# Performance work log

Measured on AMD Instinct MI355X. Metric: run time of the kernel, lower is better.

## Reference

```python
import jax, jax.numpy as jnp
import numpy as np

D, T, B, DEPTH, WIN, H = 1024, 2048, 4, 2, 128, 4
HD = D // H


def setup_inputs() -> dict:
    key = jax.random.key(0)
    ks = iter(jax.random.split(key, 32))
    s = D ** -0.5
    inp = {
        'x': jax.random.normal(next(ks), (B, T, D), jnp.float32),
        'ln1_s': jnp.ones((DEPTH, D)), 'ln1_b': jnp.zeros((DEPTH, D)),
        'ln2_s': jnp.ones((DEPTH, D)), 'ln2_b': jnp.zeros((DEPTH, D)),
        'ln3_s': jnp.ones((DEPTH, D)), 'ln3_b': jnp.zeros((DEPTH, D)),
        'rg_in_w': jax.random.normal(next(ks), (DEPTH, D, D)) * s,
        'rg_in_b': jnp.zeros((DEPTH, D)),
        'rg_gate_w': jax.random.normal(next(ks), (DEPTH, D, D)) * s,
        'rg_gate_b': jnp.zeros((DEPTH, D)),
        'rg_out_w': jax.random.normal(next(ks), (DEPTH, D, D)) * s,
        'rg_out_b': jnp.zeros((DEPTH, D)),
        'qkv_w': jax.random.normal(next(ks), (DEPTH, D, 3 * D)) * s,
        'qkv_b': jnp.zeros((DEPTH, 3 * D)),
        'attn_out_w': jax.random.normal(next(ks), (DEPTH, D, D)) * s,
        'attn_out_b': jnp.zeros((DEPTH, D)),
        'mlp_w1': jax.random.normal(next(ks), (DEPTH, D, 4 * D)) * s,
        'mlp_b1': jnp.zeros((DEPTH, 4 * D)),
        'mlp_w2': jax.random.normal(next(ks), (DEPTH, 4 * D, D)) * (4 * D) ** -0.5,
        'mlp_b2': jnp.zeros((DEPTH, D)),
    }
    return inp


def _ln(x, s, b):
    m = x.mean(-1, keepdims=True)
    v = ((x - m) ** 2).mean(-1, keepdims=True)
    return (x - m) / jnp.sqrt(v + 1e-5) * s + b


def _rg_lru(x, wi, bi, wg, bg, wo, bo):
    u = x @ wi + bi                      # [B,T,D]
    g = jax.nn.sigmoid(x @ wg + bg)      # [B,T,D]
    # h_t = g_t * h_{t-1} + (1-g_t) * u_t, h_{-1}=0 -> log-depth associative scan
    def comb(l, r):
        return (l[0] * r[0], r[0] * l[1] + r[1])
    _, h = jax.lax.associative_scan(comb, (g, (1.0 - g) * u), axis=1)
    return h @ wo + bo


def _local_attn(x, wqkv, bqkv, wo, bo):
    b, t, d = x.shape
    qkv = (x @ wqkv + bqkv).reshape(b, t, 3, H, HD)
    qkv = jnp.transpose(qkv, (2, 0, 3, 1, 4))  # [3,B,H,T,hd]
    q, k, v = qkv[0], qkv[1], qkv[2]
    scores = jnp.einsum('bhid,bhjd->bhij', q, k) / (HD ** 0.5)
    i = jnp.arange(t)[:, None]
    j = jnp.arange(t)[None, :]
    mask = (j <= i) & (j >= i - (WIN - 1))
    scores = jnp.where(mask, scores, -jnp.inf)
    p = jax.nn.softmax(scores, axis=-1)
    y = jnp.einsum('bhij,bhjd->bhid', p, v)
    y = jnp.transpose(y, (0, 2, 1, 3)).reshape(b, t, d)
    return y @ wo + bo


def reference(x, ln1_s, ln1_b, ln2_s, ln2_b, ln3_s, ln3_b,
              rg_in_w, rg_in_b, rg_gate_w, rg_gate_b, rg_out_w, rg_out_b,
              qkv_w, qkv_b, attn_out_w, attn_out_b,
              mlp_w1, mlp_b1, mlp_w2, mlp_b2):
    for l in range(DEPTH):
        x = x + _rg_lru(_ln(x, ln1_s[l], ln1_b[l]),
                        rg_in_w[l], rg_in_b[l], rg_gate_w[l], rg_gate_b[l],
                        rg_out_w[l], rg_out_b[l])
        x = x + _local_attn(_ln(x, ln2_s[l], ln2_b[l]),
                            qkv_w[l], qkv_b[l], attn_out_w[l], attn_out_b[l])
        h = _ln(x, ln3_s[l], ln3_b[l])
        h = jax.nn.gelu(h @ mlp_w1[l] + mlp_b1[l], approximate=False) @ mlp_w2[l] + mlp_b2[l]
        x = x + h
    return x
```

## Files before the change

### kernel.cpp

```cpp
#include <hip/hip_runtime.h>
#include <math.h>

#define DD 1024
#define TT 2048
#define BB 4
#define HH 4
#define HDIM 256
#define NLAYER 2
#define MM (BB*TT)
#define NCHUNK 32
#define CHUNK (TT/NCHUNK)

typedef unsigned short u16;
typedef __bf16 bf16x8 __attribute__((ext_vector_type(8)));
typedef float f32x4 __attribute__((ext_vector_type(4)));

__device__ __forceinline__ float b2f(u16 h) {
  unsigned u = ((unsigned)h) << 16;
  return __builtin_bit_cast(float, u);
}
__device__ __forceinline__ u16 f2b(float f) {
  unsigned u = __builtin_bit_cast(unsigned, f);
  u += 0x7fffu + ((u >> 16) & 1u);
  return (u16)(u >> 16);
}

#define GLD16(g, l) __builtin_amdgcn_global_load_lds( \
    (__attribute__((address_space(1))) void*)(void*)(g), \
    (__attribute__((address_space(3))) void*)(l), 16, 0, 0)

__device__ __forceinline__ void wg_barrier() {
  asm volatile("" ::: "memory");
  __builtin_amdgcn_s_barrier();
  asm volatile("" ::: "memory");
}
template<int N> __device__ __forceinline__ void wait_vmcnt() {
  asm volatile("s_waitcnt vmcnt(%0)" :: "i"(N) : "memory");
}

__global__ __launch_bounds__(256)
void transpose_cvt(const float* __restrict__ W, u16* __restrict__ Wt, int K, int N) {
  __shared__ float tile[32][33];
  const int n0 = blockIdx.x << 5, k0 = blockIdx.y << 5;
  const int tx = threadIdx.x, ty = threadIdx.y;
#pragma unroll
  for (int i = 0; i < 4; ++i)
    tile[ty + i*8][tx] = W[(size_t)(k0 + ty + i*8) * N + n0 + tx];
  __syncthreads();
#pragma unroll
  for (int i = 0; i < 4; ++i)
    Wt[(size_t)(n0 + ty + i*8) * K + k0 + tx] = f2b(tile[tx][ty + i*8]);
}

__global__ __launch_bounds__(256)
void ln_k(const float* __restrict__ x, const float* __restrict__ sc,
          const float* __restrict__ bi, u16* __restrict__ xn) {
  const int row = blockIdx.x;
  const int tid = threadIdx.x;
  const float4 xv = ((const float4*)(x + (size_t)row * DD))[tid];
  float s = xv.x + xv.y + xv.z + xv.w;
  float q = xv.x*xv.x + xv.y*xv.y + xv.z*xv.z + xv.w*xv.w;
#pragma unroll
  for (int o = 1; o < 64; o <<= 1) { s += __shfl_xor(s, o); q += __shfl_xor(q, o); }
  __shared__ float rs[4], rq[4];
  if ((tid & 63) == 0) { rs[tid >> 6] = s; rq[tid >> 6] = q; }
  __syncthreads();
  s = rs[0] + rs[1] + rs[2] + rs[3];
  q = rq[0] + rq[1] + rq[2] + rq[3];
  const float mean = s * (1.f / DD);
  const float var = q * (1.f / DD) - mean * mean;
  const float rstd = rsqrtf(var + 1e-5f);
  const float4 sv = ((const float4*)sc)[tid];
  const float4 bv = ((const float4*)bi)[tid];
  const u16 o0 = f2b((xv.x - mean) * rstd * sv.x + bv.x);
  const u16 o1 = f2b((xv.y - mean) * rstd * sv.y + bv.y);
  const u16 o2 = f2b((xv.z - mean) * rstd * sv.z + bv.z);
  const u16 o3 = f2b((xv.w - mean) * rstd * sv.w + bv.w);
  uint2 pk;
  pk.x = (unsigned)o0 | ((unsigned)o1 << 16);
  pk.y = (unsigned)o2 | ((unsigned)o3 << 16);
  *(uint2*)(xn + (size_t)row * DD + (tid << 2)) = pk;
}

template<int EPI, int BN>
__global__ __launch_bounds__(512)
void gemm256t(const u16* __restrict__ A, const u16* __restrict__ Wt,
              const float* __restrict__ bias, const float* __restrict__ bias2,
              float* __restrict__ outf, u16* __restrict__ outb, int K, int N) {
  constexpr int NI = BN / 64;
  constexpr int PAIR = 2 + BN / 128;
  extern __shared__ u16 lds[];
  u16* Al = lds;
  u16* Bl = lds + 32768;
  const int tid = threadIdx.x;
  const int gx = gridDim.x;
  const int nwg = gx * (int)gridDim.y;
  int lid = (int)blockIdx.y * gx + (int)blockIdx.x;
  lid = (lid & 7) * (nwg >> 3) + (lid >> 3);
  const int m0 = (lid / gx) << 8;
  const int n0 = (lid % gx) * BN;
  const int lane = tid & 63;
  const int wid = tid >> 6;
  const int wm = wid >> 2;
  const int wn = wid & 3;
  const int g = lane >> 4;
  const int lc = lane & 15;
  const int rkey = (lc >> 1) & 3;
  const int q = tid >> 2;
  const int sslot = tid & 3;
  const int skey = (q >> 1) & 3;
  const int scs = (sslot ^ skey) << 3;

  auto stage_pair = [&](int kt, int buf, int ch) {
    const int kbase = (kt << 6) + (ch << 5);
#pragma unroll
    for (int i = 0; i < 2; ++i) {
      const int row = i*128 + q;
      GLD16(A + (size_t)(m0 + row) * K + kbase + scs,
            Al + buf*16384 + ch*8192 + i*4096 + tid*8);
    }
#pragma unroll
    for (int i = 0; i < BN/128; ++i) {
      const int row = i*128 + q;
      GLD16(Wt + (size_t)(n0 + row) * K + kbase + scs,
            Bl + buf*(BN*64) + ch*(BN*32) + i*4096 + tid*8);
    }
  };

  f32x4 acc[8][NI];
#pragma unroll
  for (int i = 0; i < 8; ++i)
#pragma unroll
    for (int j = 0; j < NI; ++j)
#pragma unroll
      for (int e = 0; e < 4; ++e) acc[i][j][e] = 0.f;

  const int KT = K >> 6;
  stage_pair(0, 0, 0);
  stage_pair(0, 0, 1);

  for (int kt = 0; kt < KT; ++kt) {
    const int cur = kt & 1;
    const bool more = (kt + 1 < KT);
#pragma unroll
    for (int kk = 0; kk < 2; ++kk) {
      if (kk == 0) wait_vmcnt<PAIR>();
      else if (more) wait_vmcnt<PAIR>();
      else wait_vmcnt<0>();
      wg_barrier();
      const int so = (g ^ rkey) << 3;
      const u16* Ab = Al + cur*16384 + kk*8192;
      const u16* Bb = Bl + cur*(BN*64) + kk*(BN*32);
      bf16x8 bfr[NI];
#pragma unroll
      for (int ni = 0; ni < NI; ++ni)
        bfr[ni] = *(const bf16x8*)(Bb + (wn*(NI*16) + ni*16 + lc)*32 + so);
      bf16x8 af0[4];
#pragma unroll
      for (int i = 0; i < 4; ++i)
        af0[i] = *(const bf16x8*)(Ab + (wm*128 + i*16 + lc)*32 + so);
      if (more) stage_pair(kt + 1, cur ^ 1, kk);
      __builtin_amdgcn_s_setprio(1);
#pragma unroll
      for (int i = 0; i < 4; ++i)
#pragma unroll
        for (int ni = 0; ni < NI; ++ni)
          acc[i][ni] = __builtin_amdgcn_mfma_f32_16x16x32_bf16(af0[i], bfr[ni], acc[i][ni], 0, 0, 0);
      __builtin_amdgcn_s_setprio(0);
      bf16x8 af1[4];
#pragma unroll
      for (int i = 0; i < 4; ++i)
        af1[i] = *(const bf16x8*)(Ab + (wm*128 + 64 + i*16 + lc)*32 + so);
      __builtin_amdgcn_s_setprio(1);
#pragma unroll
      for (int i = 0; i < 4; ++i)
#pragma unroll
        for (int ni = 0; ni < NI; ++ni)
          acc[4 + i][ni] = __builtin_amdgcn_mfma_f32_16x16x32_bf16(af1[i], bfr[ni], acc[4 + i][ni], 0, 0, 0);
      __builtin_amdgcn_s_setprio(0);
    }
    wg_barrier();
  }

#pragma unroll
  for (int mi = 0; mi < 8; ++mi) {
#pragma unroll
    for (int ni = 0; ni < NI; ++ni) {
      const int n = n0 + wn*(NI*16) + ni*16 + lc;
      const int mbase = m0 + wm*128 + (mi & 3)*16 + (mi >> 2)*64 + (g << 2);
      if (EPI == 4) {
        const float bia = bias[n];
        if (n < 2048) {
#pragma unroll
          for (int e = 0; e < 4; ++e)
            outb[(size_t)(mbase + e) * 2048 + n] = f2b(acc[mi][ni][e] + bia);
        } else {
          const int hh = (n - 2048) >> 8, dim = (n - 2048) & 255;
          const int bidx = mbase >> 11, t = mbase & 2047;
          const u16 a0 = f2b(acc[mi][ni][0] + bia);
          const u16 a1 = f2b(acc[mi][ni][1] + bia);
          const u16 a2 = f2b(acc[mi][ni][2] + bia);
          const u16 a3 = f2b(acc[mi][ni][3] + bia);
          uint2 pk;
          pk.x = (unsigned)a0 | ((unsigned)a1 << 16);
          pk.y = (unsigned)a2 | ((unsigned)a3 << 16);
          u16* vtp = (u16*)outf;
          *(uint2*)(vtp + ((size_t)((bidx*4 + hh)*256 + dim)) * 2048 + t) = pk;
        }
      } else if (EPI == 5) {
        const float bia = (n < 1024) ? bias[n] : bias2[n - 1024];
        u16* dst = (n < 1024) ? outb : (u16*)outf;
        const int nn = n & 1023;
#pragma unroll
        for (int e = 0; e < 4; ++e)
          dst[(size_t)(mbase + e) * 1024 + nn] = f2b(acc[mi][ni][e] + bia);
      } else if (EPI == 2) {
        const float bia = bias[n];
#pragma unroll
        for (int e = 0; e < 4; ++e) {
          const float v = acc[mi][ni][e] + bia;
          const float zc = fminf(fmaxf(1.5957691216f * (v + 0.044715f*v*v*v), -30.f), 30.f);
          outb[(size_t)(mbase + e) * N + n] = f2b(v / (1.f + __expf(-zc)));
        }
      } else {
        const float bia = bias[n];
#pragma unroll
        for (int e = 0; e < 4; ++e)
          outf[(size_t)(mbase + e) * N + n] += acc[mi][ni][e] + bia;
      }
    }
  }
}

__global__ __launch_bounds__(256)
void scan1_k(const u16* __restrict__ zpre, const u16* __restrict__ u,
             float* __restrict__ aggA, float* __restrict__ aggB) {
  const int d = blockIdx.x * 256 + threadIdx.x;
  const int c = blockIdx.y, b = blockIdx.z;
  const size_t base = ((size_t)b * TT + (size_t)c * CHUNK) * DD + d;
  float a = 1.f, acc = 0.f;
  for (int t = 0; t < CHUNK; ++t) {
    const float gl = 1.f / (1.f + __expf(-b2f(zpre[base + (size_t)t * DD])));
    const float ul = b2f(u[base + (size_t)t * DD]);
    acc = gl * acc + (1.f - gl) * ul;
    a *= gl;
  }
  const size_t o = ((size_t)b * NCHUNK + c) * DD + d;
  aggA[o] = a; aggB[o] = acc;
}

__global__ __launch_bounds__(256)
void scan2_k(const float* __restrict__ aggA, const float* __restrict__ aggB,
             float* __restrict__ carry) {
  const int idx = blockIdx.x * 256 + threadIdx.x;
  const int b = idx >> 10, d = idx & 1023;
  float h = 0.f;
  for (int c = 0; c < NCHUNK; ++c) {
    const size_t o = ((size_t)b * NCHUNK + c) * DD + d;
    carry[o] = h;
    h = aggA[o] * h + aggB[o];
  }
}

__global__ __launch_bounds__(256)
void scan3_k(const u16* __restrict__ zpre, const u16* __restrict__ u,
             const float* __restrict__ carry, u16* __restrict__ hout) {
  const int d = blockIdx.x * 256 + threadIdx.x;
  const int c = blockIdx.y, b = blockIdx.z;
  const size_t base = ((size_t)b * TT + (size_t)c * CHUNK) * DD + d;
  float h = carry[((size_t)b * NCHUNK + c) * DD + d];
  for (int t = 0; t < CHUNK; ++t) {
    const float gl = 1.f / (1.f + __expf(-b2f(zpre[base + (size_t)t * DD])));
    const float ul = b2f(u[base + (size_t)t * DD]);
    h = gl * h + (1.f - gl) * ul;
    hout[base + (size_t)t * DD] = f2b(h);
  }
}

__global__ __launch_bounds__(256)
void attn_mfma(const u16* __restrict__ qkb, const u16* __restrict__ vt,
               u16* __restrict__ y) {
  __shared__ u16 kv[16384];
  __shared__ u16 pb[4][16][200];
  const int tid = threadIdx.x;
  const int lane = tid & 63;
  const int wid = tid >> 6;
  const int g = lane >> 4;
  const int lc = lane & 15;
  const int t0 = blockIdx.x << 6;
  const int bh = blockIdx.y;
  const int bT = (bh >> 2) * TT;
  const int h = bh & 3;

  bf16x8 afq[8];
  {
    const u16* qg = qkb + (size_t)(bT + t0 + wid*16 + lc) * 2048 + h*256 + g*8;
#pragma unroll
    for (int ks = 0; ks < 8; ++ks)
      afq[ks] = __builtin_bit_cast(bf16x8, *(const uint4*)(qg + ks*32));
  }

  f32x4 sc[12];
#pragma unroll
  for (int f = 0; f < 12; ++f)
#pragma unroll
    for (int e = 0; e < 4; ++e) sc[f][e] = 0.f;

  const int koff = 1024 + h*256;
#pragma unroll
  for (int c = 0; c < 3; ++c) {
    const int j0 = t0 + (c - 2) * 64;
    if (j0 < 0) {
#pragma unroll
      for (int nt = 0; nt < 4; ++nt)
#pragma unroll
        for (int e = 0; e < 4; ++e) sc[c*4+nt][e] = -1e30f;
      continue;
    }
    __syncthreads();
    {
      const u16* kg = qkb + (size_t)(bT + j0) * 2048 + koff;
#pragma unroll
      for (int i = 0; i < 8; ++i) {
        const int o16 = i*256 + tid;
        const int slab = o16 >> 8, key = (o16 >> 2) & 63, ds = o16 & 3;
        GLD16(kg + (size_t)key*2048 + slab*32 + ds*8, kv + o16*8);
      }
    }
    __syncthreads();
#pragma unroll
    for (int nt = 0; nt < 4; ++nt) {
      f32x4 s = sc[c*4+nt];
#pragma unroll
      for (int ks = 0; ks < 8; ++ks) {
        const bf16x8 kb = *(const bf16x8*)(kv + ks*2048 + (nt*16 + lc)*32 + g*8);
        s = __builtin_amdgcn_mfma_f32_16x16x32_bf16(afq[ks], kb, s, 0, 0, 0);
      }
      sc[c*4+nt] = s;
    }
#pragma unroll
    for (int nt = 0; nt < 4; ++nt)
#pragma unroll
      for (int e = 0; e < 4; ++e) {
        const int tl = wid*16 + g*4 + e;
        const int jl = nt*16 + lc;
        const bool ok = (c == 1) || (c == 2 ? (jl <= tl) : (jl >= tl + 1));
        sc[c*4+nt][e] = ok ? sc[c*4+nt][e] * 0.0625f : -1e30f;
      }
  }

#pragma unroll
  for (int e = 0; e < 4; ++e) {
    float m = -1e30f;
#pragma unroll
    for (int f = 0; f < 12; ++f) m = fmaxf(m, sc[f][e]);
    m = fmaxf(m, __shfl_xor(m, 1)); m = fmaxf(m, __shfl_xor(m, 2));
    m = fmaxf(m, __shfl_xor(m, 4)); m = fmaxf(m, __shfl_xor(m, 8));
    float s = 0.f;
#pragma unroll
    for (int f = 0; f < 12; ++f) { const float p = __expf(sc[f][e] - m); sc[f][e] = p; s += p; }
    s += __shfl_xor(s, 1); s += __shfl_xor(s, 2);
    s += __shfl_xor(s, 4); s += __shfl_xor(s, 8);
    const float is = 1.f / s;
#pragma unroll
    for (int f = 0; f < 12; ++f) sc[f][e] *= is;
  }
#pragma unroll
  for (int c = 0; c < 3; ++c)
#pragma unroll
    for (int nt = 0; nt < 4; ++nt)
#pragma unroll
      for (int e = 0; e < 4; ++e)
        pb[wid][g*4 + e][c*64 + nt*16 + lc] = f2b(sc[c*4+nt][e]);

  f32x4 acc[16];
#pragma unroll
  for (int nt = 0; nt < 16; ++nt)
#pragma unroll
    for (int e = 0; e < 4; ++e) acc[nt][e] = 0.f;

  const u16* vg = vt + (size_t)bh * 256 * 2048;
#pragma unroll
  for (int c = 0; c < 3; ++c) {
    const int j0 = t0 + (c - 2) * 64;
    if (j0 < 0) continue;
    __syncthreads();
#pragma unroll
    for (int i = 0; i < 8; ++i) {
      const int o16 = i*256 + tid;
      const int dim = o16 >> 3, slot = o16 & 7;
      const int ss = slot ^ (dim & 7);
      GLD16(vg + (size_t)dim*2048 + j0 + ss*8, kv + o16*8);
    }
    __syncthreads();
#pragma unroll
    for (int ks = 0; ks < 2; ++ks) {
      const bf16x8 pa = *(const bf16x8*)&pb[wid][lc][(c*2 + ks)*32 + g*8];
#pragma unroll
      for (int nt = 0; nt < 16; ++nt) {
        const int dim = nt*16 + lc;
        int boff = dim*128 + ks*64 + g*16;
        boff ^= (dim & 7) << 4;
        const bf16x8 vb = *(const bf16x8*)((const char*)kv + boff);
        acc[nt] = __builtin_amdgcn_mfma_f32_16x16x32_bf16(pa, vb, acc[nt], 0, 0, 0);
      }
    }
  }

#pragma unroll
  for (int nt = 0; nt < 16; ++nt)
#pragma unroll
    for (int e = 0; e < 4; ++e) {
      const int tok = bT + t0 + wid*16 + g*4 + e;
      y[(size_t)tok * 1024 + h*256 + nt*16 + lc] = f2b(acc[nt][e]);
    }
}

extern "C" void kernel_launch(void* const* d_in, const int* in_sizes, int n_in,
                              void* d_out, int out_size, void* d_ws, size_t ws_size,
                              hipStream_t stream) {
  const float* x_in      = (const float*)d_in[0];
  const float* ln1_s     = (const float*)d_in[1];
  const float* ln1_b     = (const float*)d_in[2];
  const float* ln2_s     = (const float*)d_in[3];
  const float* ln2_b     = (const float*)d_in[4];
  const float* ln3_s     = (const float*)d_in[5];
  const float* ln3_b     = (const float*)d_in[6];
  const float* rg_in_w   = (const float*)d_in[7];
  const float* rg_in_b   = (const float*)d_in[8];
  const float* rg_gate_w = (const float*)d_in[9];
  const float* rg_gate_b = (const float*)d_in[10];
  const float* rg_out_w  = (const float*)d_in[11];
  const float* rg_out_b  = (const float*)d_in[12];
  const float* qkv_w     = (const float*)d_in[13];
  const float* qkv_b     = (const float*)d_in[14];
  const float* attn_out_w= (const float*)d_in[15];
  const float* attn_out_b= (const float*)d_in[16];
  const float* mlp_w1    = (const float*)d_in[17];
  const float* mlp_b1    = (const float*)d_in[18];
  const float* mlp_w2    = (const float*)d_in[19];
  const float* mlp_b2    = (const float*)d_in[20];

  hipFuncSetAttribute((const void*)&gemm256t<5,256>, hipFuncAttributeMaxDynamicSharedMemorySize, 131072);
  hipFuncSetAttribute((const void*)&gemm256t<4,256>, hipFuncAttributeMaxDynamicSharedMemorySize, 131072);
  hipFuncSetAttribute((const void*)&gemm256t<2,256>, hipFuncAttributeMaxDynamicSharedMemorySize, 131072);
  hipFuncSetAttribute((const void*)&gemm256t<3,128>, hipFuncAttributeMaxDynamicSharedMemorySize, 98304);

  float* x = (float*)d_out;
  char* ws = (char*)d_ws;
  u16*  wt     = (u16*)ws;
  u16*  xn     = (u16*)(ws + 62914560);
  char* bigS   = ws + 62914560 + 16777216;
  char* smallS = bigS + 67108864;
  float* aggA  = (float*)(smallS + 16777216);
  float* aggB  = aggA + (size_t)BB * NCHUNK * DD;
  float* carry = aggB + (size_t)BB * NCHUNK * DD;

  u16* ubuf = (u16*)bigS;
  u16* zbuf = (u16*)(bigS + 33554432);
  u16* qkb  = (u16*)bigS;
  u16* vtb  = (u16*)(bigS + 33554432);
  u16* hid  = (u16*)bigS;
  u16* hbuf = (u16*)smallS;
  u16* ybuf = (u16*)smallS;

  hipMemcpyAsync(x, x_in, (size_t)MM * DD * sizeof(float), hipMemcpyDeviceToDevice, stream);

  const size_t LW = 15728640;
  const dim3 tb(32, 8);
  for (int l = 0; l < NLAYER; ++l) {
    u16* base = wt + (size_t)l * LW;
    transpose_cvt<<<dim3(32, 32),  tb, 0, stream>>>(rg_in_w   + (size_t)l*DD*DD,   base + 0,        DD, DD);
    transpose_cvt<<<dim3(32, 32),  tb, 0, stream>>>(rg_gate_w + (size_t)l*DD*DD,   base + 1048576,  DD, DD);
    transpose_cvt<<<dim3(32, 32),  tb, 0, stream>>>(rg_out_w  + (size_t)l*DD*DD,   base + 2097152,  DD, DD);
    transpose_cvt<<<dim3(96, 32),  tb, 0, stream>>>(qkv_w     + (size_t)l*DD*3072, base + 3145728,  DD, 3072);
    transpose_cvt<<<dim3(32, 32),  tb, 0, stream>>>(attn_out_w+ (size_t)l*DD*DD,   base + 6291456,  DD, DD);
    transpose_cvt<<<dim3(128, 32), tb, 0, stream>>>(mlp_w1    + (size_t)l*DD*4096, base + 7340032,  DD, 4096);
    transpose_cvt<<<dim3(32, 128), tb, 0, stream>>>(mlp_w2    + (size_t)l*4096*DD, base + 11534336, 4096, DD);
  }

  for (int l = 0; l < NLAYER; ++l) {
    u16* base = wt + (size_t)l * LW;
    ln_k<<<MM, 256, 0, stream>>>(x, ln1_s + l*DD, ln1_b + l*DD, xn);
    gemm256t<5,256><<<dim3(8, 32), 512, 131072, stream>>>(xn, base + 0, rg_in_b + l*DD, rg_gate_b + l*DD,
                                                          (float*)zbuf, ubuf, DD, 2048);
    scan1_k<<<dim3(4, NCHUNK, BB), 256, 0, stream>>>(zbuf, ubuf, aggA, aggB);
    scan2_k<<<16, 256, 0, stream>>>(aggA, aggB, carry);
    scan3_k<<<dim3(4, NCHUNK, BB), 256, 0, stream>>>(zbuf, ubuf, carry, hbuf);
    gemm256t<3,128><<<dim3(8, 32), 512, 98304, stream>>>(hbuf, base + 2097152, rg_out_b + l*DD, nullptr,
                                                         x, nullptr, DD, 1024);
    ln_k<<<MM, 256, 0, stream>>>(x, ln2_s + l*DD, ln2_b + l*DD, xn);
    gemm256t<4,256><<<dim3(12, 32), 512, 131072, stream>>>(xn, base + 3145728, qkv_b + l*3072, nullptr,
                                                           (float*)vtb, qkb, DD, 3072);
    attn_mfma<<<dim3(TT/64, BB*HH), 256, 0, stream>>>(qkb, vtb, ybuf);
    gemm256t<3,128><<<dim3(8, 32), 512, 98304, stream>>>(ybuf, base + 6291456, attn_out_b + l*DD, nullptr,
                                                         x, nullptr, DD, 1024);
    ln_k<<<MM, 256, 0, stream>>>(x, ln3_s + l*DD, ln3_b + l*DD, xn);
    gemm256t<2,256><<<dim3(16, 32), 512, 131072, stream>>>(xn, base + 7340032, mlp_b1 + l*4096, nullptr,
                                                           nullptr, hid, DD, 4096);
    gemm256t<3,128><<<dim3(8, 32), 512, 98304, stream>>>(hid, base + 11534336, mlp_b2 + l*DD, nullptr,
                                                         x, nullptr, 4096, 1024);
  }
}
```

Measured before the change: 910.5 us.

## Software-pipeline GEMM LDS fragment reads one K-half ahead with deeper prefetch

Restructures the GEMM main loop around K half-chunks. It prefetches three global stages up front and loads the A0/B register fragments for the next half-chunk before running the MFMAs of the current one, using double-buffered register sets. It also drops the trailing per-iteration barrier. The aim is to hide LDS read latency and global load waits behind MFMA work, at the cost of more VGPRs and a more delicate buffer-reuse and barrier ordering.

```diff
diff --git a/kernel.cpp b/kernel.cpp
--- a/kernel.cpp
+++ b/kernel.cpp
@@ -110,8 +110,10 @@
   const int sslot = tid & 3;
   const int skey = (q >> 1) & 3;
   const int scs = (sslot ^ skey) << 3;
-
-  auto stage_pair = [&](int kt, int buf, int ch) {
+  const int so = (g ^ rkey) << 3;
+
+  auto stage_pairP = [&](int p) {
+    const int kt = p >> 1, buf = kt & 1, ch = p & 1;
     const int kbase = (kt << 6) + (ch << 5);
 #pragma unroll
     for (int i = 0; i < 2; ++i) {
@@ -126,6 +128,24 @@
             Bl + buf*(BN*64) + ch*(BN*32) + i*4096 + tid*8);
     }
   };
+  auto read_b = [&](int p, bf16x8* bf) {
+    const u16* Bb = Bl + ((p >> 1) & 1)*(BN*64) + (p & 1)*(BN*32);
+#pragma unroll
+    for (int ni = 0; ni < NI; ++ni)
+      bf[ni] = *(const bf16x8*)(Bb + (wn*(NI*16) + ni*16 + lc)*32 + so);
+  };
+  auto read_a0 = [&](int p, bf16x8* af) {
+    const u16* Ab = Al + ((p >> 1) & 1)*16384 + (p & 1)*8192;
+#pragma unroll
+    for (int i = 0; i < 4; ++i)
+      af[i] = *(const bf16x8*)(Ab + (wm*128 + i*16 + lc)*32 + so);
+  };
+  auto read_a1 = [&](int p, bf16x8* af) {
+    const u16* Ab = Al + ((p >> 1) & 1)*16384 + (p & 1)*8192;
+#pragma unroll
+    for (int i = 0; i < 4; ++i)
+      af[i] = *(const bf16x8*)(Ab + (wm*128 + 64 + i*16 + lc)*32 + so);
+  };
 
   f32x4 acc[8][NI];
 #pragma unroll
@@ -136,50 +156,58 @@
       for (int e = 0; e < 4; ++e) acc[i][j][e] = 0.f;
 
   const int KT = K >> 6;
-  stage_pair(0, 0, 0);
-  stage_pair(0, 0, 1);
-
-  for (int kt = 0; kt < KT; ++kt) {
-    const int cur = kt & 1;
-    const bool more = (kt + 1 < KT);
-#pragma unroll
-    for (int kk = 0; kk < 2; ++kk) {
-      if (kk == 0) wait_vmcnt<PAIR>();
-      else if (more) wait_vmcnt<PAIR>();
-      else wait_vmcnt<0>();
+  const int NP = KT << 1;
+  stage_pairP(0); stage_pairP(1); stage_pairP(2);
+  wait_vmcnt<2*PAIR>();
+  wg_barrier();
+  bf16x8 afX[4], bfX[NI], afY[4], bfY[NI], af1[4];
+  read_a0(0, afX); read_b(0, bfX);
+
+  for (int P = 0; P < NP; P += 2) {
+    {
+      if (P + 2 < NP) wait_vmcnt<PAIR>(); else wait_vmcnt<0>();
       wg_barrier();
-      const int so = (g ^ rkey) << 3;
-      const u16* Ab = Al + cur*16384 + kk*8192;
-      const u16* Bb = Bl + cur*(BN*64) + kk*(BN*32);
-      bf16x8 bfr[NI];
-#pragma unroll
-      for (int ni = 0; ni < NI; ++ni)
-        bfr[ni] = *(const bf16x8*)(Bb + (wn*(NI*16) + ni*16 + lc)*32 + so);
-      bf16x8 af0[4];
+      read_a0(P + 1, afY); read_b(P + 1, bfY);
+      if (P + 3 < NP) stage_pairP(P + 3);
+      __builtin_amdgcn_s_setprio(1);
 #pragma unroll
       for (int i = 0; i < 4; ++i)
-        af0[i] = *(const bf16x8*)(Ab + (wm*128 + i*16 + lc)*32 + so);
-      if (more) stage_pair(kt + 1, cur ^ 1, kk);
+#pragma unroll
+        for (int ni = 0; ni < NI; ++ni)
+          acc[i][ni] = __builtin_amdgcn_mfma_f32_16x16x32_bf16(afX[i], bfX[ni], acc[i][ni], 0, 0, 0);
+      __builtin_amdgcn_s_setprio(0);
+      read_a1(P, af1);
       __builtin_amdgcn_s_setprio(1);
 #pragma unroll
       for (int i = 0; i < 4; ++i)
 #pragma unroll
         for (int ni = 0; ni < NI; ++ni)
-          acc[i][ni] = __builtin_amdgcn_mfma_f32_16x16x32_bf16(af0[i], bfr[ni], acc[i][ni], 0, 0, 0);
+          acc[4 + i][ni] = __builtin_amdgcn_mfma_f32_16x16x32_bf16(af1[i], bfX[ni], acc[4 + i][ni], 0, 0, 0);
       __builtin_amdgcn_s_setprio(0);
-      bf16x8 af1[4];
+    }
+    {
+      if (P + 2 < NP) {
+        if (P + 3 < NP) wait_vmcnt<PAIR>(); else wait_vmcnt<0>();
+        wg_barrier();
+        read_a0(P + 2, afX); read_b(P + 2, bfX);
+        if (P + 4 < NP) stage_pairP(P + 4);
+      }
+      __builtin_amdgcn_s_setprio(1);
 #pragma unroll
       for (int i = 0; i < 4; ++i)
-        af1[i] = *(const bf16x8*)(Ab + (wm*128 + 64 + i*16 + lc)*32 + so);
+#pragma unroll
+        for (int ni = 0; ni < NI; ++ni)
+          acc[i][ni] = __builtin_amdgcn_mfma_f32_16x16x32_bf16(afY[i], bfY[ni], acc[i][ni], 0, 0, 0);
+      __builtin_amdgcn_s_setprio(0);
+      read_a1(P + 1, af1);
       __builtin_amdgcn_s_setprio(1);
 #pragma unroll
       for (int i = 0; i < 4; ++i)
 #pragma unroll
         for (int ni = 0; ni < NI; ++ni)
-          acc[4 + i][ni] = __builtin_amdgcn_mfma_f32_16x16x32_bf16(af1[i], bfr[ni], acc[4 + i][ni], 0, 0, 0);
+          acc[4 + i][ni] = __builtin_amdgcn_mfma_f32_16x16x32_bf16(af1[i], bfY[ni], acc[4 + i][ni], 0, 0, 0);
       __builtin_amdgcn_s_setprio(0);
     }
-    wg_barrier();
   }
 
 #pragma unroll
```

Measured after the change: 910.3 us. About the same (-0.0%).

## Software-pipeline GEMM LDS reads with register double-buffering and batch weight transposes

Applied to the files above, without the earlier changes.

The GEMM main loop is restructured into half-k-tile phases. The next phase's A/B fragments are read from LDS into a second register set while MFMAs run on the current set, and global prefetch now runs three phases ahead. This aims to hide LDS read latency behind the matrix ops, at the cost of about twice as many fragment registers, which risks spills or lower occupancy. Separately, the per-layer weight transpose launches are merged into one launch per weight using a z grid dimension, which cuts the transpose launch count from fourteen to seven.

```diff
diff --git a/kernel.cpp b/kernel.cpp
--- a/kernel.cpp
+++ b/kernel.cpp
@@ -39,17 +39,20 @@
 }
 
 __global__ __launch_bounds__(256)
-void transpose_cvt(const float* __restrict__ W, u16* __restrict__ Wt, int K, int N) {
+void transpose_cvt(const float* __restrict__ W, u16* __restrict__ Wt, int K, int N,
+                   size_t lsrc, size_t ldst) {
   __shared__ float tile[32][33];
+  const float* Wl = W + (size_t)blockIdx.z * lsrc;
+  u16* Wtl = Wt + (size_t)blockIdx.z * ldst;
   const int n0 = blockIdx.x << 5, k0 = blockIdx.y << 5;
   const int tx = threadIdx.x, ty = threadIdx.y;
 #pragma unroll
   for (int i = 0; i < 4; ++i)
-    tile[ty + i*8][tx] = W[(size_t)(k0 + ty + i*8) * N + n0 + tx];
+    tile[ty + i*8][tx] = Wl[(size_t)(k0 + ty + i*8) * N + n0 + tx];
   __syncthreads();
 #pragma unroll
   for (int i = 0; i < 4; ++i)
-    Wt[(size_t)(n0 + ty + i*8) * K + k0 + tx] = f2b(tile[tx][ty + i*8]);
+    Wtl[(size_t)(n0 + ty + i*8) * K + k0 + tx] = f2b(tile[tx][ty + i*8]);
 }
 
 __global__ __launch_bounds__(256)
@@ -110,8 +113,10 @@
   const int sslot = tid & 3;
   const int skey = (q >> 1) & 3;
   const int scs = (sslot ^ skey) << 3;
-
-  auto stage_pair = [&](int kt, int buf, int ch) {
+  const int so = (g ^ rkey) << 3;
+
+  auto stage_pairP = [&](int p) {
+    const int kt = p >> 1, buf = kt & 1, ch = p & 1;
     const int kbase = (kt << 6) + (ch << 5);
 #pragma unroll
     for (int i = 0; i < 2; ++i) {
@@ -126,6 +131,19 @@
             Bl + buf*(BN*64) + ch*(BN*32) + i*4096 + tid*8);
     }
   };
+  auto read_set = [&](int p, bf16x8* af, bf16x8* bf) {
+    const u16* Ab = Al + ((p >> 1) & 1)*16384 + (p & 1)*8192;
+    const u16* Bb = Bl + ((p >> 1) & 1)*(BN*64) + (p & 1)*(BN*32);
+#pragma unroll
+    for (int ni = 0; ni < NI; ++ni)
+      bf[ni] = *(const bf16x8*)(Bb + (wn*(NI*16) + ni*16 + lc)*32 + so);
+#pragma unroll
+    for (int i = 0; i < 4; ++i)
+      af[i] = *(const bf16x8*)(Ab + (wm*128 + i*16 + lc)*32 + so);
+#pragma unroll
+    for (int i = 0; i < 4; ++i)
+      af[4 + i] = *(const bf16x8*)(Ab + (wm*128 + 64 + i*16 + lc)*32 + so);
+  };
 
   f32x4 acc[8][NI];
 #pragma unroll
@@ -136,51 +154,37 @@
       for (int e = 0; e < 4; ++e) acc[i][j][e] = 0.f;
 
   const int KT = K >> 6;
-  stage_pair(0, 0, 0);
-  stage_pair(0, 0, 1);
-
-  for (int kt = 0; kt < KT; ++kt) {
-    const int cur = kt & 1;
-    const bool more = (kt + 1 < KT);
-#pragma unroll
-    for (int kk = 0; kk < 2; ++kk) {
-      if (kk == 0) wait_vmcnt<PAIR>();
-      else if (more) wait_vmcnt<PAIR>();
-      else wait_vmcnt<0>();
-      wg_barrier();
-      const int so = (g ^ rkey) << 3;
-      const u16* Ab = Al + cur*16384 + kk*8192;
-      const u16* Bb = Bl + cur*(BN*64) + kk*(BN*32);
-      bf16x8 bfr[NI];
-#pragma unroll
-      for (int ni = 0; ni < NI; ++ni)
-        bfr[ni] = *(const bf16x8*)(Bb + (wn*(NI*16) + ni*16 + lc)*32 + so);
-      bf16x8 af0[4];
-#pragma unroll
-      for (int i = 0; i < 4; ++i)
-        af0[i] = *(const bf16x8*)(Ab + (wm*128 + i*16 + lc)*32 + so);
-      if (more) stage_pair(kt + 1, cur ^ 1, kk);
-      __builtin_amdgcn_s_setprio(1);
-#pragma unroll
-      for (int i = 0; i < 4; ++i)
-#pragma unroll
-        for (int ni = 0; ni < NI; ++ni)
-          acc[i][ni] = __builtin_amdgcn_mfma_f32_16x16x32_bf16(af0[i], bfr[ni], acc[i][ni], 0, 0, 0);
-      __builtin_amdgcn_s_setprio(0);
-      bf16x8 af1[4];
-#pragma unroll
-      for (int i = 0; i < 4; ++i)
-        af1[i] = *(const bf16x8*)(Ab + (wm*128 + 64 + i*16 + lc)*32 + so);
-      __builtin_amdgcn_s_setprio(1);
-#pragma unroll
-      for (int i = 0; i < 4; ++i)
-#pragma unroll
-        for (int ni = 0; ni < NI; ++ni)
-          acc[4 + i][ni] = __builtin_amdgcn_mfma_f32_16x16x32_bf16(af1[i], bfr[ni], acc[4 + i][ni], 0, 0, 0);
-      __builtin_amdgcn_s_setprio(0);
-    }
-    wg_barrier();
-  }
+  const int NP = KT << 1;
+  stage_pairP(0); stage_pairP(1); stage_pairP(2);
+  wait_vmcnt<2*PAIR>();
+  wg_barrier();
+  bf16x8 afX[8], bfX[NI], afY[8], bfY[NI];
+  read_set(0, afX, bfX);
+
+#define GPHASE(PP, CURA, CURB, NXTA, NXTB)                                          \
+  {                                                                                 \
+    const int P_ = (PP);                                                            \
+    if (P_ + 1 < NP) {                                                              \
+      if (P_ + 2 < NP) wait_vmcnt<PAIR>(); else wait_vmcnt<0>();                    \
+      wg_barrier();                                                                 \
+      read_set(P_ + 1, NXTA, NXTB);                                                 \
+      if (P_ + 3 < NP) stage_pairP(P_ + 3);                                         \
+    }                                                                               \
+    __builtin_amdgcn_s_setprio(1);                                                  \
+    _Pragma("unroll")                                                               \
+    for (int i = 0; i < 8; ++i)                                                     \
+      _Pragma("unroll")                                                             \
+      for (int ni = 0; ni < NI; ++ni)                                               \
+        acc[i][ni] = __builtin_amdgcn_mfma_f32_16x16x32_bf16(CURA[i], CURB[ni],     \
+                                                             acc[i][ni], 0, 0, 0); \
+    __builtin_amdgcn_s_setprio(0);                                                  \
+  }
+
+  for (int P = 0; P < NP; P += 2) {
+    GPHASE(P,     afX, bfX, afY, bfY)
+    GPHASE(P + 1, afY, bfY, afX, bfX)
+  }
+#undef GPHASE
 
 #pragma unroll
   for (int mi = 0; mi < 8; ++mi) {
@@ -468,16 +472,13 @@
 
   const size_t LW = 15728640;
   const dim3 tb(32, 8);
-  for (int l = 0; l < NLAYER; ++l) {
-    u16* base = wt + (size_t)l * LW;
-    transpose_cvt<<<dim3(32, 32),  tb, 0, stream>>>(rg_in_w   + (size_t)l*DD*DD,   base + 0,        DD, DD);
-    transpose_cvt<<<dim3(32, 32),  tb, 0, stream>>>(rg_gate_w + (size_t)l*DD*DD,   base + 1048576,  DD, DD);
-    transpose_cvt<<<dim3(32, 32),  tb, 0, stream>>>(rg_out_w  + (size_t)l*DD*DD,   base + 2097152,  DD, DD);
-    transpose_cvt<<<dim3(96, 32),  tb, 0, stream>>>(qkv_w     + (size_t)l*DD*3072, base + 3145728,  DD, 3072);
-    transpose_cvt<<<dim3(32, 32),  tb, 0, stream>>>(attn_out_w+ (size_t)l*DD*DD,   base + 6291456,  DD, DD);
-    transpose_cvt<<<dim3(128, 32), tb, 0, stream>>>(mlp_w1    + (size_t)l*DD*4096, base + 7340032,  DD, 4096);
-    transpose_cvt<<<dim3(32, 128), tb, 0, stream>>>(mlp_w2    + (size_t)l*4096*DD, base + 11534336, 4096, DD);
-  }
+  transpose_cvt<<<dim3(32, 32, 2),  tb, 0, stream>>>(rg_in_w,    wt + 0,        DD, DD,   DD*DD,   LW);
+  transpose_cvt<<<dim3(32, 32, 2),  tb, 0, stream>>>(rg_gate_w,  wt + 1048576,  DD, DD,   DD*DD,   LW);
+  transpose_cvt<<<dim3(32, 32, 2),  tb, 0, stream>>>(rg_out_w,   wt + 2097152,  DD, DD,   DD*DD,   LW);
+  transpose_cvt<<<dim3(96, 32, 2),  tb, 0, stream>>>(qkv_w,      wt + 3145728,  DD, 3072, DD*3072, LW);
+  transpose_cvt<<<dim3(32, 32, 2),  tb, 0, stream>>>(attn_out_w, wt + 6291456,  DD, DD,   DD*DD,   LW);
+  transpose_cvt<<<dim3(128, 32, 2), tb, 0, stream>>>(mlp_w1,     wt + 7340032,  DD, 4096, DD*4096, LW);
+  transpose_cvt<<<dim3(32, 128, 2), tb, 0, stream>>>(mlp_w2,     wt + 11534336, 4096, DD, 4096*DD, LW);
 
   for (int l = 0; l < NLAYER; ++l) {
     u16* base = wt + (size_t)l * LW;
```

Result: no change. 900.5 us (-1.1%).
